# Kernel tuning notes

Measured on AMD Instinct MI355X. Metric: run time of the kernel, lower is better.

The kernel has to match this reference:

```python
import jax, jax.numpy as jnp
import numpy as np

DEGREE = 8


def _askey_wilson_basis(x, a, b, c, d, q, degree):
    # Iterative 3-term recurrence (same math as the recursive torch version).
    # x: (batch, input_dim); a,b,c,d,q: scalars broadcast over x.
    basis = [jnp.ones_like(x)]
    if degree >= 1:
        p1 = (2 * (1 + a * b * q) * x - (a + b) * (1 + c * d * q)) / (1 + a * b * c * d * q ** 2)
        basis.append(p1)
    for n in range(2, degree + 1):
        An = (1 - a * b * q ** (n - 1)) * (1 - c * d * q ** (n - 1)) * (1 - a * b * c * d * q ** (2 * n - 2))
        An = An / ((1 - a * b * c * d * q ** (2 * n - 1)) * (1 - a * b * c * d * q ** (2 * n)))
        Cn = (1 - q ** n) * (1 - a * b * q ** (n - 1)) * (1 - c * d * q ** (n - 1)) * (1 - a * b * c * d * q ** (2 * n - 2))
        Cn = Cn / ((1 - a * b * c * d * q ** (2 * n - 2)) * (1 - a * b * c * d * q ** (2 * n - 1)))
        pn = ((2 * x - An) * basis[n - 1] - Cn * basis[n - 2]) / (1 - q ** n)
        basis.append(pn)
    return jnp.stack(basis, axis=-1)  # (batch, input_dim, degree+1)


def setup_inputs() -> dict:
    key = jax.random.key(0)
    k1, k2, k3, k4, k5, k6, k7 = jax.random.split(key, 7)
    input_dim, output_dim, degree = 1024, 1024, DEGREE
    batch = 8192
    x = jax.random.normal(k1, (batch, input_dim), dtype=jnp.float32)
    a = jax.random.normal(k2, (1,), dtype=jnp.float32)
    b = jax.random.normal(k3, (1,), dtype=jnp.float32)
    c = jax.random.normal(k4, (1,), dtype=jnp.float32)
    d = jax.random.normal(k5, (1,), dtype=jnp.float32)
    q = jax.random.normal(k6, (1,), dtype=jnp.float32)
    std = 1.0 / (input_dim * (degree + 1))
    coeffs = jax.random.normal(k7, (input_dim, output_dim, degree + 1), dtype=jnp.float32) * std
    return {"x": x, "a": a, "b": b, "c": c, "d": d, "q": q, "coeffs": coeffs}


def reference(x, a, b, c, d, q, coeffs) -> jnp.ndarray:
    a0, b0, c0, d0, q0 = a[0], b[0], c[0], d[0], q[0]
    basis = _askey_wilson_basis(x, a0, b0, c0, d0, q0, DEGREE)  # (b, i, d+1)
    y = jnp.einsum('bid,iod->bo', basis, coeffs)
    return y
```

## Files before the change

### kernel.cpp

```cpp
#include <hip/hip_runtime.h>
#include <cstdint>

typedef unsigned short u16;
typedef __bf16 bf16x8 __attribute__((ext_vector_type(8)));
typedef float f32x4 __attribute__((ext_vector_type(4)));

#define M_DIM 8192
#define N_DIM 1024
#define I_DIM 1024
#define NDEG 8
#define K_DIM (I_DIM * NDEG)
#define BM 256
#define BN 128
#define BK 64
#define NT (K_DIM / BK)
#define A_TILE (BM * BK)
#define B_TILE (BN * BK)

__device__ __forceinline__ u16 f2bf(float f) {
    union { float f; uint32_t u; } v; v.f = f;
    return (u16)((v.u + 0x7FFFu + ((v.u >> 16) & 1u)) >> 16);
}

__device__ __forceinline__ void gload_lds16(const u16* g, u16* l) {
    auto lp = reinterpret_cast<__attribute__((address_space(3))) uint32_t*>(
        reinterpret_cast<uintptr_t>(l));
    __builtin_amdgcn_global_load_lds(reinterpret_cast<const uint32_t*>(g), lp, 16, 0, 0);
}

__global__ __launch_bounds__(256) void aw_transform(
    const float* __restrict__ coeffs, u16* __restrict__ Bt, float* __restrict__ bias)
{
    __shared__ float lds[32][292];
    int bi = blockIdx.x >> 5, bo = blockIdx.x & 31;
    int i0 = bi * 32, o0 = bo * 32;
    int t = threadIdx.x;

    {
        int r = t >> 3, s = t & 7;
        const float4* src = (const float4*)(coeffs + ((size_t)(i0 + r) * N_DIM + o0) * 9);
#pragma unroll
        for (int j = 0; j < 9; ++j) {
            float4 v = src[s * 9 + j];
            *(float4*)&lds[r][(s * 9 + j) * 4] = v;
        }
    }
    __syncthreads();

    {
        int c = t >> 3, s2 = t & 7;
        u16 ob[32];
#pragma unroll
        for (int rr = 0; rr < 4; ++rr)
#pragma unroll
            for (int dd = 0; dd < 8; ++dd)
                ob[rr * 8 + dd] = f2bf(lds[s2 * 4 + rr][c * 9 + 1 + dd]);
        uint4* dst = (uint4*)(Bt + (size_t)(o0 + c) * K_DIM + (size_t)i0 * 8 + s2 * 32);
        const uint4* sp = (const uint4*)ob;
#pragma unroll
        for (int u = 0; u < 4; ++u) dst[u] = sp[u];
    }

    if (t < 32) {
        float sum = 0.f;
#pragma unroll
        for (int rr = 0; rr < 32; ++rr) sum += lds[rr][t * 9];
        atomicAdd(&bias[o0 + t], sum);
    }
}

__global__ void aw_basis(const float* __restrict__ x,
                         const float* __restrict__ pa, const float* __restrict__ pb,
                         const float* __restrict__ pc, const float* __restrict__ pd,
                         const float* __restrict__ pq,
                         u16* __restrict__ A, int row0)
{
    int t  = blockIdx.x * 256 + threadIdx.x;
    int rb = t >> 7;
    int g  = t & 127;
    int i0 = g << 3;
    int b  = row0 + rb;

    float a = *pa, bb = *pb, c = *pc, d = *pd, q = *pq;
    float ab = a * bb, cd = c * d, abcd = ab * cd;

    float qp[17];
    qp[0] = 1.f;
#pragma unroll
    for (int k = 1; k <= 16; ++k) qp[k] = qp[k - 1] * q;

    float den1 = 1.f + abcd * q * q;
    float c1x = 2.f * (1.f + ab * q) / den1;
    float c1c = -(a + bb) * (1.f + cd * q) / den1;

    float An[9], Cn[9], Sn[9];
#pragma unroll
    for (int n = 2; n <= 8; ++n) {
        float t1 = 1.f - ab * qp[n - 1];
        float t2 = 1.f - cd * qp[n - 1];
        float t3 = 1.f - abcd * qp[2 * n - 2];
        float t4 = 1.f - abcd * qp[2 * n - 1];
        float t5 = 1.f - abcd * qp[2 * n];
        An[n] = (t1 * t2 * t3) / (t4 * t5);
        Cn[n] = ((1.f - qp[n]) * t1 * t2 * t3) / (t3 * t4);
        Sn[n] = 1.f / (1.f - qp[n]);
    }

    const float4* x4 = (const float4*)(x + (size_t)b * I_DIM + i0);
    float4 v0 = x4[0], v1 = x4[1];
    float xv[8] = {v0.x, v0.y, v0.z, v0.w, v1.x, v1.y, v1.z, v1.w};

    u16 ob[64];
#pragma unroll
    for (int j = 0; j < 8; ++j) {
        float xj = xv[j];
        float p1 = c1x * xj + c1c;
        ob[j * 8 + 0] = f2bf(p1);
        float pm2 = 1.f, pm1 = p1;
#pragma unroll
        for (int n = 2; n <= 8; ++n) {
            float pn = ((2.f * xj - An[n]) * pm1 - Cn[n] * pm2) * Sn[n];
            ob[j * 8 + n - 1] = f2bf(pn);
            pm2 = pm1; pm1 = pn;
        }
    }

    uint4* dst = (uint4*)(A + (size_t)rb * K_DIM + (size_t)i0 * 8);
    const uint4* s = (const uint4*)ob;
#pragma unroll
    for (int u = 0; u < 8; ++u) dst[u] = s[u];
}

__global__ __launch_bounds__(512) void aw_gemm(
    const u16* __restrict__ A,
    const u16* __restrict__ B,
    const float* __restrict__ bias,
    float* __restrict__ C,
    int row0, int rowBlocks)
{
    __shared__ u16 As[3 * A_TILE];
    __shared__ u16 Bs[3 * B_TILE];

    int nwg = rowBlocks * 8;
    int bid = blockIdx.x;
    int per = nwg >> 3;
    int logical = (bid & 7) * per + (bid >> 3);
    int rowBlk = logical >> 3;
    int colBlk = logical & 7;

    const int tid  = threadIdx.x;
    const int lane = tid & 63;
    const int wid  = tid >> 6;
    const int wr = wid & 3;
    const int wc = wid >> 2;

    const size_t aBase = (size_t)rowBlk * BM * K_DIM;
    const size_t bBase = (size_t)colBlk * BN * K_DIM;

    f32x4 acc[4][4];
#pragma unroll
    for (int mi = 0; mi < 4; ++mi)
#pragma unroll
        for (int ni = 0; ni < 4; ++ni)
            acc[mi][ni] = (f32x4){0.f, 0.f, 0.f, 0.f};

    auto stage = [&](int kt, int buf) {
        const int k0 = kt * BK;
        u16* dA = As + buf * A_TILE;
        u16* dB = Bs + buf * B_TILE;
#pragma unroll
        for (int j = 0; j < 4; ++j) {
            int idx = j * 512 + tid;
            int r = idx >> 3, sl = idx & 7;
            int col = (sl ^ (r & 7)) << 3;
            gload_lds16(A + aBase + (size_t)r * K_DIM + k0 + col, dA + (idx << 3));
        }
#pragma unroll
        for (int j = 0; j < 2; ++j) {
            int idx = j * 512 + tid;
            int r = idx >> 3, sl = idx & 7;
            int col = (sl ^ (r & 7)) << 3;
            gload_lds16(B + bBase + (size_t)r * K_DIM + k0 + col, dB + (idx << 3));
        }
    };

    auto compute = [&](int buf) {
        const char* aB = (const char*)(As + buf * A_TILE);
        const char* bB = (const char*)(Bs + buf * B_TILE);
#pragma unroll
        for (int ks = 0; ks < 2; ++ks) {
            bf16x8 af[4], bfr[4];
#pragma unroll
            for (int mi = 0; mi < 4; ++mi) {
                int r = wr * 64 + mi * 16 + (lane & 15);
                int s = ks * 4 + (lane >> 4);
                af[mi] = *(const bf16x8*)(aB + r * 128 + ((s ^ (r & 7)) << 4));
            }
#pragma unroll
            for (int ni = 0; ni < 4; ++ni) {
                int r = wc * 64 + ni * 16 + (lane & 15);
                int s = ks * 4 + (lane >> 4);
                bfr[ni] = *(const bf16x8*)(bB + r * 128 + ((s ^ (r & 7)) << 4));
            }
            __builtin_amdgcn_s_setprio(1);
#pragma unroll
            for (int mi = 0; mi < 4; ++mi)
#pragma unroll
                for (int ni = 0; ni < 4; ++ni)
                    acc[mi][ni] = __builtin_amdgcn_mfma_f32_16x16x32_bf16(
                        af[mi], bfr[ni], acc[mi][ni], 0, 0, 0);
            __builtin_amdgcn_s_setprio(0);
        }
    };

    stage(0, 0);
    stage(1, 1);

    for (int t = 0; t < NT; ++t) {
        __builtin_amdgcn_s_barrier();
        if (t + 2 < NT) {
            stage(t + 2, (t + 2) % 3);
            asm volatile("s_waitcnt vmcnt(12)" ::: "memory");
        } else if (t + 1 < NT) {
            asm volatile("s_waitcnt vmcnt(6)" ::: "memory");
        } else {
            asm volatile("s_waitcnt vmcnt(0)" ::: "memory");
        }
        __builtin_amdgcn_s_barrier();
        compute(t % 3);
    }

    int gRow = row0 + rowBlk * BM + wr * 64;
    int gCol = colBlk * BN + wc * 64;
#pragma unroll
    for (int mi = 0; mi < 4; ++mi) {
#pragma unroll
        for (int ni = 0; ni < 4; ++ni) {
            int rr = gRow + mi * 16 + ((lane >> 4) << 2);
            int cc = gCol + ni * 16 + (lane & 15);
            float bv = bias[cc];
            float* dst = C + (size_t)rr * N_DIM + cc;
#pragma unroll
            for (int j = 0; j < 4; ++j) dst[(size_t)j * N_DIM] = acc[mi][ni][j] + bv;
        }
    }
}

extern "C" void kernel_launch(void* const* d_in, const int* in_sizes, int n_in,
                              void* d_out, int out_size, void* d_ws, size_t ws_size,
                              hipStream_t stream)
{
    const float* x      = (const float*)d_in[0];
    const float* pa     = (const float*)d_in[1];
    const float* pb     = (const float*)d_in[2];
    const float* pc     = (const float*)d_in[3];
    const float* pd     = (const float*)d_in[4];
    const float* pq     = (const float*)d_in[5];
    const float* coeffs = (const float*)d_in[6];
    float* out = (float*)d_out;

    float* bias = (float*)d_ws;
    const size_t biasBytes = 4096;
    u16* Bt = (u16*)((char*)d_ws + biasBytes);
    const size_t btBytes = (size_t)N_DIM * K_DIM * sizeof(u16);
    u16* Abuf = (u16*)((char*)d_ws + biasBytes + btBytes);
    size_t used = biasBytes + btBytes;
    size_t avail = ws_size > used ? ws_size - used : 0;

    int chunk = M_DIM;
    while (chunk > 256 && (size_t)chunk * K_DIM * sizeof(u16) > avail) chunk >>= 1;

    hipMemsetAsync(bias, 0, N_DIM * sizeof(float), stream);
    aw_transform<<<1024, 256, 0, stream>>>(coeffs, Bt, bias);

    for (int row0 = 0; row0 < M_DIM; row0 += chunk) {
        aw_basis<<<(chunk * 128) / 256, 256, 0, stream>>>(x, pa, pb, pc, pd, pq, Abuf, row0);
        int rowBlocks = chunk / BM;
        aw_gemm<<<rowBlocks * 8, 512, 0, stream>>>(Abuf, Bt, bias, out, row0, rowBlocks);
    }
}
```

Baseline: 197.4 us.

## Interleave half-tile prefetches with MFMA k-steps and precompute load addresses

Restructures the main GEMM loop so each k-tile is processed as two k-steps, with half of the next-next tile's global-to-LDS loads issued between LDS fragment reads and MFMA blocks. Global and LDS addresses are precomputed once into per-thread pointers and offsets, which removes per-iteration index arithmetic. Barriers now separate the half-stages, and the wait counts are adjusted to the three-load halves. The aim is to spread memory issue across compute and cut address overhead, at the cost of extra barriers and register pressure from the stored pointers and offsets.

```diff
diff --git a/kernel.cpp b/kernel.cpp
--- a/kernel.cpp
+++ b/kernel.cpp
@@ -154,8 +154,39 @@
     const int wr = wid & 3;
     const int wc = wid >> 2;
 
-    const size_t aBase = (size_t)rowBlk * BM * K_DIM;
-    const size_t bBase = (size_t)colBlk * BN * K_DIM;
+    const u16* gA[4]; const u16* gB[2];
+    int ldsA[4], ldsB[2];
+#pragma unroll
+    for (int j = 0; j < 4; ++j) {
+        int idx = j * 512 + tid;
+        int r = idx >> 3, sl = idx & 7;
+        gA[j] = A + (size_t)rowBlk * BM * K_DIM + (size_t)r * K_DIM + ((sl ^ (r & 7)) << 3);
+        ldsA[j] = idx << 3;
+    }
+#pragma unroll
+    for (int j = 0; j < 2; ++j) {
+        int idx = j * 512 + tid;
+        int r = idx >> 3, sl = idx & 7;
+        gB[j] = B + (size_t)colBlk * BN * K_DIM + (size_t)r * K_DIM + ((sl ^ (r & 7)) << 3);
+        ldsB[j] = idx << 3;
+    }
+
+    int offA[2][4], offB[2][4];
+#pragma unroll
+    for (int ks = 0; ks < 2; ++ks) {
+#pragma unroll
+        for (int mi = 0; mi < 4; ++mi) {
+            int r = wr * 64 + mi * 16 + (lane & 15);
+            int s = ks * 4 + (lane >> 4);
+            offA[ks][mi] = r * 128 + ((s ^ (r & 7)) << 4);
+        }
+#pragma unroll
+        for (int ni = 0; ni < 4; ++ni) {
+            int r = wc * 64 + ni * 16 + (lane & 15);
+            int s = ks * 4 + (lane >> 4);
+            offB[ks][ni] = r * 128 + ((s ^ (r & 7)) << 4);
+        }
+    }
 
     f32x4 acc[4][4];
 #pragma unroll
@@ -164,70 +195,70 @@
         for (int ni = 0; ni < 4; ++ni)
             acc[mi][ni] = (f32x4){0.f, 0.f, 0.f, 0.f};
 
-    auto stage = [&](int kt, int buf) {
+    auto stageHalf = [&](int kt, int buf, int half) {
         const int k0 = kt * BK;
         u16* dA = As + buf * A_TILE;
         u16* dB = Bs + buf * B_TILE;
-#pragma unroll
-        for (int j = 0; j < 4; ++j) {
-            int idx = j * 512 + tid;
-            int r = idx >> 3, sl = idx & 7;
-            int col = (sl ^ (r & 7)) << 3;
-            gload_lds16(A + aBase + (size_t)r * K_DIM + k0 + col, dA + (idx << 3));
-        }
-#pragma unroll
-        for (int j = 0; j < 2; ++j) {
-            int idx = j * 512 + tid;
-            int r = idx >> 3, sl = idx & 7;
-            int col = (sl ^ (r & 7)) << 3;
-            gload_lds16(B + bBase + (size_t)r * K_DIM + k0 + col, dB + (idx << 3));
+        if (half == 0) {
+            gload_lds16(gA[0] + k0, dA + ldsA[0]);
+            gload_lds16(gA[1] + k0, dA + ldsA[1]);
+            gload_lds16(gB[0] + k0, dB + ldsB[0]);
+        } else {
+            gload_lds16(gA[2] + k0, dA + ldsA[2]);
+            gload_lds16(gA[3] + k0, dA + ldsA[3]);
+            gload_lds16(gB[1] + k0, dB + ldsB[1]);
         }
     };
 
-    auto compute = [&](int buf) {
+    stageHalf(0, 0, 0); stageHalf(0, 0, 1);
+    stageHalf(1, 1, 0); stageHalf(1, 1, 1);
+    asm volatile("s_waitcnt vmcnt(6)" ::: "memory");
+    __builtin_amdgcn_s_barrier();
+
+    int buf = 0;
+    for (int t = 0; t < NT; ++t) {
         const char* aB = (const char*)(As + buf * A_TILE);
         const char* bB = (const char*)(Bs + buf * B_TILE);
-#pragma unroll
-        for (int ks = 0; ks < 2; ++ks) {
-            bf16x8 af[4], bfr[4];
-#pragma unroll
-            for (int mi = 0; mi < 4; ++mi) {
-                int r = wr * 64 + mi * 16 + (lane & 15);
-                int s = ks * 4 + (lane >> 4);
-                af[mi] = *(const bf16x8*)(aB + r * 128 + ((s ^ (r & 7)) << 4));
-            }
-#pragma unroll
-            for (int ni = 0; ni < 4; ++ni) {
-                int r = wc * 64 + ni * 16 + (lane & 15);
-                int s = ks * 4 + (lane >> 4);
-                bfr[ni] = *(const bf16x8*)(bB + r * 128 + ((s ^ (r & 7)) << 4));
-            }
-            __builtin_amdgcn_s_setprio(1);
-#pragma unroll
-            for (int mi = 0; mi < 4; ++mi)
-#pragma unroll
-                for (int ni = 0; ni < 4; ++ni)
-                    acc[mi][ni] = __builtin_amdgcn_mfma_f32_16x16x32_bf16(
-                        af[mi], bfr[ni], acc[mi][ni], 0, 0, 0);
-            __builtin_amdgcn_s_setprio(0);
-        }
-    };
-
-    stage(0, 0);
-    stage(1, 1);
-
-    for (int t = 0; t < NT; ++t) {
+        int nb = buf + 2; if (nb >= 3) nb -= 3;
+        const bool pf = (t + 2 < NT);
+
+        bf16x8 a0[4], b0[4];
+#pragma unroll
+        for (int mi = 0; mi < 4; ++mi) a0[mi] = *(const bf16x8*)(aB + offA[0][mi]);
+#pragma unroll
+        for (int ni = 0; ni < 4; ++ni) b0[ni] = *(const bf16x8*)(bB + offB[0][ni]);
+        if (pf) stageHalf(t + 2, nb, 0);
         __builtin_amdgcn_s_barrier();
-        if (t + 2 < NT) {
-            stage(t + 2, (t + 2) % 3);
-            asm volatile("s_waitcnt vmcnt(12)" ::: "memory");
-        } else if (t + 1 < NT) {
-            asm volatile("s_waitcnt vmcnt(6)" ::: "memory");
-        } else {
-            asm volatile("s_waitcnt vmcnt(0)" ::: "memory");
-        }
+        __builtin_amdgcn_s_setprio(1);
+#pragma unroll
+        for (int mi = 0; mi < 4; ++mi)
+#pragma unroll
+            for (int ni = 0; ni < 4; ++ni)
+                acc[mi][ni] = __builtin_amdgcn_mfma_f32_16x16x32_bf16(
+                    a0[mi], b0[ni], acc[mi][ni], 0, 0, 0);
+        __builtin_amdgcn_s_setprio(0);
         __builtin_amdgcn_s_barrier();
-        compute(t % 3);
+
+        bf16x8 a1[4], b1[4];
+#pragma unroll
+        for (int mi = 0; mi < 4; ++mi) a1[mi] = *(const bf16x8*)(aB + offA[1][mi]);
+#pragma unroll
+        for (int ni = 0; ni < 4; ++ni) b1[ni] = *(const bf16x8*)(bB + offB[1][ni]);
+        if (pf) stageHalf(t + 2, nb, 1);
+        __builtin_amdgcn_s_barrier();
+        __builtin_amdgcn_s_setprio(1);
+#pragma unroll
+        for (int mi = 0; mi < 4; ++mi)
+#pragma unroll
+            for (int ni = 0; ni < 4; ++ni)
+                acc[mi][ni] = __builtin_amdgcn_mfma_f32_16x16x32_bf16(
+                    a1[mi], b1[ni], acc[mi][ni], 0, 0, 0);
+        __builtin_amdgcn_s_setprio(0);
+        if (pf) { asm volatile("s_waitcnt vmcnt(6)" ::: "memory"); }
+        else if (t + 1 < NT) { asm volatile("s_waitcnt vmcnt(0)" ::: "memory"); }
+        __builtin_amdgcn_s_barrier();
+
+        buf += 1; if (buf >= 3) buf -= 3;
     }
 
     int gRow = row0 + rowBlk * BM + wr * 64;
```

Measured after the change: 190.3 us. 3.6% less time.

## Restructure GEMM main loop into 4-stage pipeline with register double-buffered fragments

Applied to the files above, without the earlier changes.

Halves the K tile to 32, grows the LDS ring to four stages, and software-pipelines LDS fragment reads into alternating register sets so the next tile's ds_reads overlap the current tile's MFMAs. Global load addresses and LDS read offsets are precomputed once, with a 4-slot XOR swizzle suited to 64-byte rows. It also adds a launch bounds hint of two workgroups per CU and uses one barrier per tile instead of two. The cost is more barriers per unit of work because tiles are smaller, plus higher register pressure from the double-buffered fragments.

```diff
diff --git a/kernel.cpp b/kernel.cpp
--- a/kernel.cpp
+++ b/kernel.cpp
@@ -12,7 +12,7 @@
 #define K_DIM (I_DIM * NDEG)
 #define BM 256
 #define BN 128
-#define BK 64
+#define BK 32
 #define NT (K_DIM / BK)
 #define A_TILE (BM * BK)
 #define B_TILE (BN * BK)
@@ -131,15 +131,15 @@
     for (int u = 0; u < 8; ++u) dst[u] = s[u];
 }
 
-__global__ __launch_bounds__(512) void aw_gemm(
+__global__ __launch_bounds__(512, 2) void aw_gemm(
     const u16* __restrict__ A,
     const u16* __restrict__ B,
     const float* __restrict__ bias,
     float* __restrict__ C,
     int row0, int rowBlocks)
 {
-    __shared__ u16 As[3 * A_TILE];
-    __shared__ u16 Bs[3 * B_TILE];
+    __shared__ alignas(16) u16 As[4 * A_TILE];
+    __shared__ alignas(16) u16 Bs[4 * B_TILE];
 
     int nwg = rowBlocks * 8;
     int bid = blockIdx.x;
@@ -154,8 +154,38 @@
     const int wr = wid & 3;
     const int wc = wid >> 2;
 
-    const size_t aBase = (size_t)rowBlk * BM * K_DIM;
-    const size_t bBase = (size_t)colBlk * BN * K_DIM;
+    const u16 *gA0, *gA1, *gB0;
+    int ldsA0, ldsA1, ldsB0;
+    {
+        const size_t aBase = (size_t)rowBlk * BM * K_DIM;
+        const size_t bBase = (size_t)colBlk * BN * K_DIM;
+        int idx = tid;
+        int r = idx >> 2, sl = idx & 3;
+        gA0 = A + aBase + (size_t)r * K_DIM + (((sl ^ (r & 3) ^ ((r >> 2) & 3)) & 3) << 3);
+        ldsA0 = idx << 3;
+        idx = 512 + tid;
+        r = idx >> 2; sl = idx & 3;
+        gA1 = A + aBase + (size_t)r * K_DIM + (((sl ^ (r & 3) ^ ((r >> 2) & 3)) & 3) << 3);
+        ldsA1 = idx << 3;
+        idx = tid;
+        r = idx >> 2; sl = idx & 3;
+        gB0 = B + bBase + (size_t)r * K_DIM + (((sl ^ (r & 3) ^ ((r >> 2) & 3)) & 3) << 3);
+        ldsB0 = idx << 3;
+    }
+
+    int offA[4], offB[4];
+#pragma unroll
+    for (int mi = 0; mi < 4; ++mi) {
+        int r = wr * 64 + mi * 16 + (lane & 15);
+        int s = lane >> 4;
+        offA[mi] = r * 64 + (((s ^ (r & 3) ^ ((r >> 2) & 3)) & 3) << 4);
+    }
+#pragma unroll
+    for (int ni = 0; ni < 4; ++ni) {
+        int r = wc * 64 + ni * 16 + (lane & 15);
+        int s = lane >> 4;
+        offB[ni] = r * 64 + (((s ^ (r & 3) ^ ((r >> 2) & 3)) & 3) << 4);
+    }
 
     f32x4 acc[4][4];
 #pragma unroll
@@ -168,67 +198,55 @@
         const int k0 = kt * BK;
         u16* dA = As + buf * A_TILE;
         u16* dB = Bs + buf * B_TILE;
-#pragma unroll
-        for (int j = 0; j < 4; ++j) {
-            int idx = j * 512 + tid;
-            int r = idx >> 3, sl = idx & 7;
-            int col = (sl ^ (r & 7)) << 3;
-            gload_lds16(A + aBase + (size_t)r * K_DIM + k0 + col, dA + (idx << 3));
-        }
-#pragma unroll
-        for (int j = 0; j < 2; ++j) {
-            int idx = j * 512 + tid;
-            int r = idx >> 3, sl = idx & 7;
-            int col = (sl ^ (r & 7)) << 3;
-            gload_lds16(B + bBase + (size_t)r * K_DIM + k0 + col, dB + (idx << 3));
-        }
+        gload_lds16(gA0 + k0, dA + ldsA0);
+        gload_lds16(gA1 + k0, dA + ldsA1);
+        gload_lds16(gB0 + k0, dB + ldsB0);
     };
-
-    auto compute = [&](int buf) {
+    auto rdfrags = [&](bf16x8 (&fa)[4], bf16x8 (&fb)[4], int buf) {
         const char* aB = (const char*)(As + buf * A_TILE);
         const char* bB = (const char*)(Bs + buf * B_TILE);
 #pragma unroll
-        for (int ks = 0; ks < 2; ++ks) {
-            bf16x8 af[4], bfr[4];
-#pragma unroll
-            for (int mi = 0; mi < 4; ++mi) {
-                int r = wr * 64 + mi * 16 + (lane & 15);
-                int s = ks * 4 + (lane >> 4);
-                af[mi] = *(const bf16x8*)(aB + r * 128 + ((s ^ (r & 7)) << 4));
-            }
-#pragma unroll
-            for (int ni = 0; ni < 4; ++ni) {
-                int r = wc * 64 + ni * 16 + (lane & 15);
-                int s = ks * 4 + (lane >> 4);
-                bfr[ni] = *(const bf16x8*)(bB + r * 128 + ((s ^ (r & 7)) << 4));
-            }
-            __builtin_amdgcn_s_setprio(1);
-#pragma unroll
-            for (int mi = 0; mi < 4; ++mi)
-#pragma unroll
-                for (int ni = 0; ni < 4; ++ni)
-                    acc[mi][ni] = __builtin_amdgcn_mfma_f32_16x16x32_bf16(
-                        af[mi], bfr[ni], acc[mi][ni], 0, 0, 0);
-            __builtin_amdgcn_s_setprio(0);
-        }
+        for (int mi = 0; mi < 4; ++mi) fa[mi] = *(const bf16x8*)(aB + offA[mi]);
+#pragma unroll
+        for (int ni = 0; ni < 4; ++ni) fb[ni] = *(const bf16x8*)(bB + offB[ni]);
     };
-
-    stage(0, 0);
-    stage(1, 1);
-
-    for (int t = 0; t < NT; ++t) {
-        __builtin_amdgcn_s_barrier();
-        if (t + 2 < NT) {
-            stage(t + 2, (t + 2) % 3);
-            asm volatile("s_waitcnt vmcnt(12)" ::: "memory");
-        } else if (t + 1 < NT) {
-            asm volatile("s_waitcnt vmcnt(6)" ::: "memory");
-        } else {
-            asm volatile("s_waitcnt vmcnt(0)" ::: "memory");
-        }
-        __builtin_amdgcn_s_barrier();
-        compute(t % 3);
-    }
+    auto domfma = [&](bf16x8 (&fa)[4], bf16x8 (&fb)[4]) {
+        __builtin_amdgcn_s_setprio(1);
+#pragma unroll
+        for (int mi = 0; mi < 4; ++mi)
+#pragma unroll
+            for (int ni = 0; ni < 4; ++ni)
+                acc[mi][ni] = __builtin_amdgcn_mfma_f32_16x16x32_bf16(
+                    fa[mi], fb[ni], acc[mi][ni], 0, 0, 0);
+        __builtin_amdgcn_s_setprio(0);
+    };
+
+#define TILE(CURA, CURB, NXTA, NXTB, T, DOS, DOR, VM)                         \
+    do {                                                                      \
+        if (DOS) stage((T) + 3, ((T) + 3) & 3);                               \
+        if (DOR) rdfrags(NXTA, NXTB, ((T) + 1) & 3);                          \
+        domfma(CURA, CURB);                                                   \
+        if ((VM) == 3) asm volatile("s_waitcnt vmcnt(3)" ::: "memory");       \
+        else if ((VM) == 0) asm volatile("s_waitcnt vmcnt(0)" ::: "memory");  \
+        __builtin_amdgcn_s_barrier();                                         \
+    } while (0)
+
+    stage(0, 0); stage(1, 1); stage(2, 2);
+    asm volatile("s_waitcnt vmcnt(3)" ::: "memory");
+    __builtin_amdgcn_s_barrier();
+
+    bf16x8 fa0[4], fb0[4], fa1[4], fb1[4];
+    rdfrags(fa0, fb0, 0);
+
+    for (int t = 0; t < NT - 4; t += 2) {
+        TILE(fa0, fb0, fa1, fb1, t,     true,  true, 3);
+        TILE(fa1, fb1, fa0, fb0, t + 1, true,  true, 3);
+    }
+    TILE(fa0, fb0, fa1, fb1, NT - 4, true,  true, 3);
+    TILE(fa1, fb1, fa0, fb0, NT - 3, false, true, 0);
+    TILE(fa0, fb0, fa1, fb1, NT - 2, false, true, -1);
+    domfma(fa1, fb1);
+#undef TILE
 
     int gRow = row0 + rowBlk * BM + wr * 64;
     int gCol = colBlk * BN + wc * 64;
```

Result: slower. 205.6 us (+4.2%).
